# Optimization experiments

Hardware: AMD Instinct MI355X
Metric: run time of the kernel (lower is better)

The kernel has to match this reference:

```python
import jax, jax.numpy as jnp
import numpy as np

N = 20000   # nodes
E = 320000  # directed edges (before self-loops)
D = 64      # input_dim
H = 10      # GAT heads
HD = H * D  # 640
NEG_SLOPE = 0.2


def setup_inputs() -> dict:
    key = jax.random.key(0)
    ks = jax.random.split(key, 10)
    return {
        "x": jax.random.normal(ks[0], (N, D), jnp.float32),
        "W_gat": jax.random.normal(ks[1], (D, HD), jnp.float32) / np.sqrt(D).astype(np.float32),
        "att_src": jax.random.normal(ks[2], (H, D), jnp.float32) / np.sqrt(D).astype(np.float32),
        "att_dst": jax.random.normal(ks[3], (H, D), jnp.float32) / np.sqrt(D).astype(np.float32),
        "b_gat": jnp.zeros((HD,), jnp.float32),
        "W_gcn": jax.random.normal(ks[4], (HD, HD), jnp.float32) / np.sqrt(HD).astype(np.float32),
        "b_gcn": jnp.zeros((HD,), jnp.float32),
        "W1": jax.random.normal(ks[5], (2 * HD, 1500), jnp.float32) / np.sqrt(2 * HD).astype(np.float32),
        "b1": jnp.zeros((1500,), jnp.float32),
        "W2": jax.random.normal(ks[6], (1500, 10), jnp.float32) / np.sqrt(1500).astype(np.float32),
        "b2": jnp.zeros((10,), jnp.float32),
        "edge_index": jax.random.randint(ks[7], (2, E), 0, N, dtype=jnp.int64),
    }


def _forward(x, W_gat, att_src, att_dst, b_gat, W_gcn, b_gcn, W1, b1, W2, b2, edge_index):
    n = x.shape[0]
    # add self-loops (PyG default for both GATConv and GCNConv)
    loop = jnp.arange(n, dtype=edge_index.dtype)
    ei = jnp.concatenate([edge_index, jnp.stack([loop, loop])], axis=1)
    src, dst = ei[0], ei[1]

    # ---- GATConv(D -> D, heads=H, concat) ----
    xl = (x @ W_gat).reshape(n, H, D)                      # [N,H,D]
    a_src = jnp.einsum('nhd,hd->nh', xl, att_src)          # [N,H]
    a_dst = jnp.einsum('nhd,hd->nh', xl, att_dst)          # [N,H]
    alpha = jax.nn.leaky_relu(a_src[src] + a_dst[dst], NEG_SLOPE)  # [E',H]
    m = jax.ops.segment_max(alpha, dst, num_segments=n)    # segment softmax over incoming edges
    ex = jnp.exp(alpha - m[dst])
    den = jax.ops.segment_sum(ex, dst, num_segments=n)
    w = ex / (den[dst] + 1e-16)                            # [E',H]
    msg = xl[src] * w[:, :, None]                          # [E',H,D]
    x1 = jax.ops.segment_sum(msg, dst, num_segments=n).reshape(n, HD) + b_gat
    x1 = jax.nn.relu(x1)

    # ---- GCNConv(HD -> HD), symmetric norm with self-loops ----
    deg = jax.ops.segment_sum(jnp.ones(ei.shape[1], x.dtype), dst, num_segments=n)
    dinv = jnp.where(deg > 0, jax.lax.rsqrt(deg), 0.0)
    norm = dinv[src] * dinv[dst]                           # [E']
    xw = x1 @ W_gcn                                        # [N,HD]
    x2 = jax.ops.segment_sum(xw[src] * norm[:, None], dst, num_segments=n) + b_gcn
    x2 = jax.nn.relu(x2)

    # ---- global max/mean pool (batch=None -> single graph) + MLP head ----
    pooled = jnp.concatenate([x2.max(axis=0, keepdims=True),
                              x2.mean(axis=0, keepdims=True)], axis=1)  # [1, 2*HD]
    h = jax.nn.relu(pooled @ W1 + b1)
    # dropout is identity in eval mode
    return h @ W2 + b2                                     # [1, 10]


def reference(x, W_gat, att_src, att_dst, b_gat, W_gcn, b_gcn, W1, b1, W2, b2, edge_index):
    return _forward(x, W_gat, att_src, att_dst, b_gat, W_gcn, b_gcn, W1, b1, W2, b2, edge_index)
```

## Files before the change

kernel.cpp:

```cpp
#include <hip/hip_runtime.h>
#include <hip/hip_bf16.h>
#include <math.h>

#define NN 20000
#define DD 64
#define HH 10
#define HDIM 640
#define NEG 0.2f
#define H1 1500
#define BKK 128

typedef _Float16 half8 __attribute__((ext_vector_type(8)));
typedef _Float16 half4v __attribute__((ext_vector_type(4)));
typedef float f32x4 __attribute__((ext_vector_type(4)));

__global__ __launch_bounds__(256) void k_cvtB(const float* __restrict__ Wgcn,
                                              const float* __restrict__ Wg,
                                              _Float16* __restrict__ Wbt,
                                              _Float16* __restrict__ WgT)
{
    __shared__ float t[32][33];
    const int bx = blockIdx.x;
    int by = blockIdx.y;
    const float* W; _Float16* WT; int rows, cols;
    if (by < 20) { W = Wgcn; WT = Wbt; rows = HDIM; cols = HDIM; }
    else         { W = Wg;   WT = WgT; rows = DD;   cols = HDIM; by -= 20; }
    const int lx = threadIdx.x & 31, ly = threadIdx.x >> 5;
    #pragma unroll
    for (int i = ly; i < 32; i += 8)
        t[i][lx] = W[(size_t)(by * 32 + i) * cols + bx * 32 + lx];
    __syncthreads();
    #pragma unroll
    for (int j = ly; j < 32; j += 8)
        WT[(size_t)(bx * 32 + j) * rows + by * 32 + lx] = (_Float16)t[lx][j];
}

__global__ __launch_bounds__(256) void k_gemm1(
    const float* __restrict__ x, const _Float16* __restrict__ WgT,
    const float* __restrict__ att_s, const float* __restrict__ att_d,
    _Float16* __restrict__ xl, float* __restrict__ aST, float* __restrict__ aDT)
{
    __shared__ _Float16 As[128][72];
    __shared__ _Float16 Bs[64][72];
    const int tid = threadIdx.x;
    const int m0 = blockIdx.x * 128;
    const int h  = blockIdx.y;
    const int n0 = h * 64;

    {
        const int row = tid >> 1, ch = (tid & 1) * 32;
        const int gr = m0 + row;
        if (gr < NN) {
            const float* xp = &x[(size_t)gr * DD + ch];
            #pragma unroll
            for (int i = 0; i < 8; ++i) {
                const float4 v = *(const float4*)&xp[i * 4];
                half4v o = {(_Float16)v.x, (_Float16)v.y, (_Float16)v.z, (_Float16)v.w};
                *(half4v*)&As[row][ch + i * 4] = o;
            }
        } else {
            const half8 z = {0, 0, 0, 0, 0, 0, 0, 0};
            #pragma unroll
            for (int i = 0; i < 4; ++i) *(half8*)&As[row][ch + i * 8] = z;
        }
    }
    {
        const int row = tid >> 2, part = (tid & 3) * 16;
        const _Float16* wp = &WgT[(size_t)(n0 + row) * DD + part];
        *(half8*)&Bs[row][part]     = *(const half8*)&wp[0];
        *(half8*)&Bs[row][part + 8] = *(const half8*)&wp[8];
    }
    __syncthreads();

    const int lane = tid & 63, wave = tid >> 6;
    const int l15 = lane & 15, quad = lane >> 4;
    f32x4 acc[2][4];
    #pragma unroll
    for (int r = 0; r < 2; ++r)
        #pragma unroll
        for (int c = 0; c < 4; ++c) acc[r][c] = (f32x4){0.f, 0.f, 0.f, 0.f};

    #pragma unroll
    for (int ks = 0; ks < 2; ++ks) {
        const half8 a0 = *(const half8*)&As[wave * 32 + l15][ks * 32 + quad * 8];
        const half8 a1 = *(const half8*)&As[wave * 32 + 16 + l15][ks * 32 + quad * 8];
        #pragma unroll
        for (int c = 0; c < 4; ++c) {
            const half8 b = *(const half8*)&Bs[c * 16 + l15][ks * 32 + quad * 8];
            acc[0][c] = __builtin_amdgcn_mfma_f32_16x16x32_f16(a0, b, acc[0][c], 0, 0, 0);
            acc[1][c] = __builtin_amdgcn_mfma_f32_16x16x32_f16(a1, b, acc[1][c], 0, 0, 0);
        }
    }

    float asv[4], adv[4];
    #pragma unroll
    for (int c = 0; c < 4; ++c) {
        asv[c] = att_s[h * DD + c * 16 + l15];
        adv[c] = att_d[h * DD + c * 16 + l15];
    }
    #pragma unroll
    for (int r = 0; r < 2; ++r) {
        float ps[4] = {0.f, 0.f, 0.f, 0.f}, pd[4] = {0.f, 0.f, 0.f, 0.f};
        #pragma unroll
        for (int c = 0; c < 4; ++c)
            #pragma unroll
            for (int g = 0; g < 4; ++g) {
                ps[g] = fmaf(acc[r][c][g], asv[c], ps[g]);
                pd[g] = fmaf(acc[r][c][g], adv[c], pd[g]);
            }
        #pragma unroll
        for (int m = 1; m <= 8; m <<= 1)
            #pragma unroll
            for (int g = 0; g < 4; ++g) {
                ps[g] += __shfl_xor(ps[g], m);
                pd[g] += __shfl_xor(pd[g], m);
            }
        #pragma unroll
        for (int c = 0; c < 4; ++c)
            #pragma unroll
            for (int g = 0; g < 4; ++g) {
                const int row = m0 + wave * 32 + r * 16 + quad * 4 + g;
                if (row < NN)
                    xl[(size_t)row * HDIM + n0 + c * 16 + l15] = (_Float16)acc[r][c][g];
            }
        if (l15 == 0)
            #pragma unroll
            for (int g = 0; g < 4; ++g) {
                const int row = m0 + wave * 32 + r * 16 + quad * 4 + g;
                if (row < NN) {
                    aST[(size_t)h * NN + row] = ps[g];
                    aDT[(size_t)h * NN + row] = pd[g];
                }
            }
    }
}

__global__ void k_count(const int* __restrict__ ei, int E, int* __restrict__ cnt)
{
    const int e = blockIdx.x * blockDim.x + threadIdx.x;
    if (e >= E + NN) return;
    const int d = (e < E) ? ei[E + e] : (e - E);
    atomicAdd(&cnt[d], 1);
}

__global__ __launch_bounds__(1024) void k_scan(const int* __restrict__ cnt,
                                               int* __restrict__ rowptr,
                                               float* __restrict__ dinv)
{
    __shared__ int sh[1024];
    const int t = threadIdx.x;
    const int CH = 20;
    const int base = t * CH;
    int loc[CH];
    int s = 0;
    #pragma unroll
    for (int i = 0; i < CH; ++i) {
        const int idx = base + i;
        const int c = (idx < NN) ? cnt[idx] : 0;
        loc[i] = s; s += c;
    }
    sh[t] = s; __syncthreads();
    for (int off = 1; off < 1024; off <<= 1) {
        const int v = (t >= off) ? sh[t - off] : 0;
        __syncthreads();
        sh[t] += v;
        __syncthreads();
    }
    const int prev = (t == 0) ? 0 : sh[t - 1];
    #pragma unroll
    for (int i = 0; i < CH; ++i) {
        const int idx = base + i;
        if (idx < NN) {
            rowptr[idx] = prev + loc[i];
            dinv[idx]   = rsqrtf((float)cnt[idx]);
        }
    }
    if (t == 1023) rowptr[NN] = sh[1023];
}

__global__ void k_fill(const int* __restrict__ ei, int E,
                       const int* __restrict__ rowptr,
                       int* __restrict__ cursor, int* __restrict__ csr)
{
    const int e = blockIdx.x * blockDim.x + threadIdx.x;
    if (e >= E + NN) return;
    int s, d;
    if (e < E) { s = ei[e]; d = ei[E + e]; } else { s = d = e - E; }
    const int pos = atomicAdd(&cursor[d], 1);
    csr[rowptr[d] + pos] = s;
}

__device__ __forceinline__ bool slice_map3(int bid, int& s, int& m)
{
    const int r = bid & 7, k = bid >> 3;
    if (k < 625) { s = r; m = k; return true; }
    s = 8 + (r >> 2);
    m = (r & 3) * 157 + (k - 625);
    return m < 625;
}

__device__ __forceinline__ float lrexp(float a)
{
    a = (a >= 0.f) ? a : NEG * a;
    return __expf(a);
}

__global__ __launch_bounds__(256) void k_gat_gather4(
    const int* __restrict__ rowptr, const int* __restrict__ csr,
    const float* __restrict__ aST, const float* __restrict__ aDT,
    const _Float16* __restrict__ xl, const float* __restrict__ b_gat,
    _Float16* __restrict__ x1)
{
    int s, m;
    if (!slice_map3(blockIdx.x, s, m)) return;
    const int wave = threadIdx.x >> 6, lane = threadIdx.x & 63;
    const int g = lane >> 3, l = lane & 7;
    const int n = m * 32 + wave * 8 + g;
    const int col = s * 64 + l * 8;
    const float* __restrict__ as = aST + (size_t)s * NN;
    const _Float16* __restrict__ xc = xl + col;
    const float ad = aDT[(size_t)s * NN + n];

    float acc[8];
    #pragma unroll
    for (int i = 0; i < 8; ++i) acc[i] = 0.f;
    float ws = 0.f;

    const int j0 = rowptr[n], j1 = rowptr[n + 1];
    int j = j0;
    for (; j + 3 < j1; j += 4) {
        const int sA = csr[j], sB = csr[j + 1], sC = csr[j + 2], sD = csr[j + 3];
        const float wA = lrexp(as[sA] + ad);
        const float wB = lrexp(as[sB] + ad);
        const float wC = lrexp(as[sC] + ad);
        const float wD = lrexp(as[sD] + ad);
        ws += wA + wB + wC + wD;
        const half8 vA = *(const half8*)&xc[(size_t)sA * HDIM];
        const half8 vB = *(const half8*)&xc[(size_t)sB * HDIM];
        const half8 vC = *(const half8*)&xc[(size_t)sC * HDIM];
        const half8 vD = *(const half8*)&xc[(size_t)sD * HDIM];
        #pragma unroll
        for (int i = 0; i < 8; ++i) {
            acc[i] = fmaf(wA, (float)vA[i], acc[i]);
            acc[i] = fmaf(wB, (float)vB[i], acc[i]);
            acc[i] = fmaf(wC, (float)vC[i], acc[i]);
            acc[i] = fmaf(wD, (float)vD[i], acc[i]);
        }
    }
    for (; j < j1; ++j) {
        const int sA = csr[j];
        const float wA = lrexp(as[sA] + ad);
        ws += wA;
        const half8 vA = *(const half8*)&xc[(size_t)sA * HDIM];
        #pragma unroll
        for (int i = 0; i < 8; ++i) acc[i] = fmaf(wA, (float)vA[i], acc[i]);
    }

    const float rr = 1.f / (ws + 1e-16f);
    const float4 ba = *(const float4*)&b_gat[col];
    const float4 bb = *(const float4*)&b_gat[col + 4];
    const float bv[8] = {ba.x, ba.y, ba.z, ba.w, bb.x, bb.y, bb.z, bb.w};
    half8 o;
    #pragma unroll
    for (int i = 0; i < 8; ++i) {
        const float v = fmaf(acc[i], rr, bv[i]);
        o[i] = (_Float16)((v > 0.f) ? v : 0.f);
    }
    *(half8*)&x1[(size_t)n * HDIM + col] = o;
}

__global__ __launch_bounds__(256) void k_gcn_gather4(
    const int* __restrict__ rowptr, const int* __restrict__ csr,
    const float* __restrict__ dinv, const _Float16* __restrict__ x1,
    _Float16* __restrict__ t)
{
    int s, m;
    if (!slice_map3(blockIdx.x, s, m)) return;
    const int wave = threadIdx.x >> 6, lane = threadIdx.x & 63;
    const int g = lane >> 3, l = lane & 7;
    const int n = m * 32 + wave * 8 + g;
    const int col = s * 64 + l * 8;
    const _Float16* __restrict__ xc = x1 + col;
    const float dd = dinv[n];

    float acc[8];
    #pragma unroll
    for (int i = 0; i < 8; ++i) acc[i] = 0.f;

    const int j0 = rowptr[n], j1 = rowptr[n + 1];
    int j = j0;
    for (; j + 3 < j1; j += 4) {
        const int sA = csr[j], sB = csr[j + 1], sC = csr[j + 2], sD = csr[j + 3];
        const float wA = dinv[sA] * dd, wB = dinv[sB] * dd;
        const float wC = dinv[sC] * dd, wD = dinv[sD] * dd;
        const half8 vA = *(const half8*)&xc[(size_t)sA * HDIM];
        const half8 vB = *(const half8*)&xc[(size_t)sB * HDIM];
        const half8 vC = *(const half8*)&xc[(size_t)sC * HDIM];
        const half8 vD = *(const half8*)&xc[(size_t)sD * HDIM];
        #pragma unroll
        for (int i = 0; i < 8; ++i) {
            acc[i] = fmaf(wA, (float)vA[i], acc[i]);
            acc[i] = fmaf(wB, (float)vB[i], acc[i]);
            acc[i] = fmaf(wC, (float)vC[i], acc[i]);
            acc[i] = fmaf(wD, (float)vD[i], acc[i]);
        }
    }
    for (; j < j1; ++j) {
        const int sA = csr[j];
        const float wA = dinv[sA] * dd;
        const half8 vA = *(const half8*)&xc[(size_t)sA * HDIM];
        #pragma unroll
        for (int i = 0; i < 8; ++i) acc[i] = fmaf(wA, (float)vA[i], acc[i]);
    }

    half8 o;
    #pragma unroll
    for (int i = 0; i < 8; ++i) o[i] = (_Float16)acc[i];
    *(half8*)&t[(size_t)n * HDIM + col] = o;
}

__global__ __launch_bounds__(256) void k_gemm2(const _Float16* __restrict__ X,
                                               const _Float16* __restrict__ Wbt,
                                               const float* __restrict__ b_gcn,
                                               float* __restrict__ pmax,
                                               float* __restrict__ psum)
{
    __shared__ _Float16 Bs[2][128 * BKK];
    const int bid = blockIdx.x;
    const int r = bid & 7, q = bid >> 3;
    const int strip = (q / 5) * 8 + r;
    const int nt = q % 5;
    if (strip >= 157) return;

    const int tid = threadIdx.x;
    const int lane = tid & 63, wave = tid >> 6;
    const int l15 = lane & 15, quad = lane >> 4;
    const int m0 = strip * 128 + wave * 32;
    const int n0 = nt * 128;
    const int l7 = l15 & 7;
    const int jrow = lane >> 4, jchunk = lane & 15;

    f32x4 acc[2][8];
    #pragma unroll
    for (int rr = 0; rr < 2; ++rr)
        #pragma unroll
        for (int c = 0; c < 8; ++c) acc[rr][c] = (f32x4){0.f, 0.f, 0.f, 0.f};

    const _Float16* a0p = &X[(size_t)(m0 + l15) * HDIM + quad * 8];
    const _Float16* a1p = a0p + (size_t)16 * HDIM;

#define STAGE2(buf, kb)                                                          \
    {                                                                            \
        _Pragma("unroll")                                                        \
        for (int i = 0; i < 8; ++i) {                                            \
            const int rw = (wave * 8 + i) * 4 + jrow;                            \
            const int ck = jchunk ^ (rw & 7);                                    \
            const _Float16* src = &Wbt[(size_t)(n0 + rw) * HDIM + (kb) + ck * 8];\
            __builtin_amdgcn_global_load_lds(                                    \
                (const __attribute__((address_space(1))) void*)src,              \
                (__attribute__((address_space(3))) void*)&Bs[buf][(size_t)(wave * 8 + i) * 512], \
                16, 0, 0);                                                       \
        }                                                                        \
    }

    STAGE2(0, 0);
    for (int it = 0; it < 5; ++it) {
        const int kb = it * BKK;
        half8 a0[4], a1[4];
        #pragma unroll
        for (int ks = 0; ks < 4; ++ks) {
            a0[ks] = *(const half8*)(a0p + kb + ks * 32);
            a1[ks] = *(const half8*)(a1p + kb + ks * 32);
        }
        if (it < 4) {
            STAGE2((it + 1) & 1, kb + BKK);
            asm volatile("s_waitcnt vmcnt(8)" ::: "memory");
        } else {
            asm volatile("s_waitcnt vmcnt(0)" ::: "memory");
        }
        __builtin_amdgcn_s_barrier();
        const _Float16* Bsc = Bs[it & 1];
        #pragma unroll
        for (int ks = 0; ks < 4; ++ks) {
            #pragma unroll
            for (int c = 0; c < 8; ++c) {
                const int br = c * 16 + l15;
                const int ck = (4 * ks + quad) ^ l7;
                const half8 b = *(const half8*)&Bsc[(size_t)br * BKK + ck * 8];
                acc[0][c] = __builtin_amdgcn_mfma_f32_16x16x32_f16(a0[ks], b, acc[0][c], 0, 0, 0);
                acc[1][c] = __builtin_amdgcn_mfma_f32_16x16x32_f16(a1[ks], b, acc[1][c], 0, 0, 0);
            }
        }
        __builtin_amdgcn_s_barrier();
    }
#undef STAGE2

    float lmax[8], lsum[8];
    #pragma unroll
    for (int c = 0; c < 8; ++c) { lmax[c] = 0.f; lsum[c] = 0.f; }
    #pragma unroll
    for (int c = 0; c < 8; ++c) {
        const float bb = b_gcn[n0 + c * 16 + l15];
        #pragma unroll
        for (int rr = 0; rr < 2; ++rr)
            #pragma unroll
            for (int g = 0; g < 4; ++g) {
                const int row = m0 + rr * 16 + quad * 4 + g;
                if (row < NN) {
                    float v = acc[rr][c][g] + bb;
                    v = (v > 0.f) ? v : 0.f;
                    lmax[c] = fmaxf(lmax[c], v);
                    lsum[c] += v;
                }
            }
    }
    float* redm = (float*)Bs;
    float* reds = redm + 128;
    if (tid < 128) { redm[tid] = 0.f; reds[tid] = 0.f; }
    __syncthreads();
    #pragma unroll
    for (int c = 0; c < 8; ++c) {
        const int col = c * 16 + l15;
        atomicMax((int*)&redm[col], __float_as_int(lmax[c]));
        atomicAdd(&reds[col], lsum[c]);
    }
    __syncthreads();
    if (tid < 128) {
        atomicMax((int*)&pmax[n0 + tid], __float_as_int(redm[tid]));
        atomicAdd(&psum[n0 + tid], reds[tid]);
    }
}

__global__ __launch_bounds__(256) void k_mlp1(const float* __restrict__ pmax,
                                              const float* __restrict__ psum,
                                              const float* __restrict__ W1,
                                              float* __restrict__ hacc)
{
    __shared__ float pl[80];
    const int t = threadIdx.x;
    const int i0 = blockIdx.y * 80;
    if (t < 80) {
        const int i = i0 + t;
        pl[t] = (i < HDIM) ? pmax[i] : psum[i - HDIM] * (1.0f / NN);
    }
    __syncthreads();
    const int j = blockIdx.x * 256 + t;
    if (j >= H1) return;
    float acc = 0.f;
    #pragma unroll 8
    for (int i = 0; i < 80; ++i)
        acc = fmaf(pl[i], W1[(size_t)(i0 + i) * H1 + j], acc);
    atomicAdd(&hacc[j], acc);
}

__global__ __launch_bounds__(256) void k_mlp2(const float* __restrict__ hacc,
                                              const float* __restrict__ b1,
                                              const float* __restrict__ W2,
                                              const float* __restrict__ b2,
                                              float* __restrict__ out)
{
    __shared__ float hsh[H1];
    __shared__ float red[256];
    const int t = threadIdx.x;
    for (int i = t; i < H1; i += 256) {
        const float v = hacc[i] + b1[i];
        hsh[i] = (v > 0.f) ? v : 0.f;
    }
    __syncthreads();
    float acc[10];
    #pragma unroll
    for (int k = 0; k < 10; ++k) acc[k] = 0.f;
    for (int i = t; i < H1; i += 256) {
        const float h = hsh[i];
        #pragma unroll
        for (int k = 0; k < 10; ++k) acc[k] = fmaf(h, W2[i * 10 + k], acc[k]);
    }
    for (int k = 0; k < 10; ++k) {
        red[t] = acc[k]; __syncthreads();
        for (int s2 = 128; s2 > 0; s2 >>= 1) {
            if (t < s2) red[t] += red[t + s2];
            __syncthreads();
        }
        if (t == 0) out[k] = red[0] + b2[k];
        __syncthreads();
    }
}

extern "C" void kernel_launch(void* const* d_in, const int* in_sizes, int n_in,
                              void* d_out, int out_size, void* d_ws, size_t ws_size,
                              hipStream_t stream)
{
    const float* x     = (const float*)d_in[0];
    const float* Wg    = (const float*)d_in[1];
    const float* att_s = (const float*)d_in[2];
    const float* att_d = (const float*)d_in[3];
    const float* b_gat = (const float*)d_in[4];
    const float* Wgcn  = (const float*)d_in[5];
    const float* b_gcn = (const float*)d_in[6];
    const float* W1    = (const float*)d_in[7];
    const float* b1    = (const float*)d_in[8];
    const float* W2    = (const float*)d_in[9];
    const float* b2    = (const float*)d_in[10];
    const int*   ei    = (const int*)d_in[11];
    const int E = in_sizes[11] / 2;
    const int EP = E + NN;
    float* out = (float*)d_out;

    char* wsp = (char*)d_ws;
    size_t off = 0;
    auto alc = [&](size_t b) { void* p = wsp + off; off += (b + 255) & ~(size_t)255; return p; };
    _Float16* bufA = (_Float16*)alc((size_t)NN * HDIM * 2);
    _Float16* bufB = (_Float16*)alc((size_t)NN * HDIM * 2);
    float* aST    = (float*)alc((size_t)HH * NN * 4);
    float* aDT    = (float*)alc((size_t)HH * NN * 4);
    int*   rowptr = (int*)alc((size_t)(NN + 1) * 4);
    int*   csr    = (int*)alc((size_t)EP * 4);
    float* dinv   = (float*)alc((size_t)NN * 4);
    _Float16* Wbt = (_Float16*)alc((size_t)HDIM * HDIM * 2);
    _Float16* WgT = (_Float16*)alc((size_t)HDIM * DD * 2);
    const size_t zoff = off;
    int*   cnt    = (int*)alc((size_t)NN * 4);
    int*   cursor = (int*)alc((size_t)NN * 4);
    float* pmax   = (float*)alc((size_t)HDIM * 4);
    float* psum   = (float*)alc((size_t)HDIM * 4);
    float* hacc   = (float*)alc((size_t)H1 * 4);
    const size_t zsize = off - zoff;

    hipMemsetAsync(cnt, 0, zsize, stream);

    dim3 gw(HDIM / 32, HDIM / 32 + DD / 32);
    k_cvtB<<<gw, 256, 0, stream>>>(Wgcn, Wg, Wbt, WgT);
    dim3 g1((NN + 127) / 128, HH);
    k_gemm1<<<g1, 256, 0, stream>>>(x, WgT, att_s, att_d, bufA, aST, aDT);
    k_count<<<(EP + 255) / 256, 256, 0, stream>>>(ei, E, cnt);
    k_scan<<<1, 1024, 0, stream>>>(cnt, rowptr, dinv);
    k_fill<<<(EP + 255) / 256, 256, 0, stream>>>(ei, E, rowptr, cursor, csr);
    const int GG = 6256;
    k_gat_gather4<<<GG, 256, 0, stream>>>(rowptr, csr, aST, aDT, bufA, b_gat, bufB);
    k_gcn_gather4<<<GG, 256, 0, stream>>>(rowptr, csr, dinv, bufB, bufA);
    k_gemm2<<<800, 256, 0, stream>>>(bufA, Wbt, b_gcn, pmax, psum);
    dim3 gm1(6, 16);
    k_mlp1<<<gm1, 256, 0, stream>>>(pmax, psum, W1, hacc);
    k_mlp2<<<1, 256, 0, stream>>>(hacc, b1, W2, b2, out);
}
```

Measured before the change: 317.4 us.

## Widen gather per-thread columns to 16 and halve GEMM K-tile

The GAT and GCN gather kernels now give each thread 16 feature columns (two half8 loads per neighbor) with 4 lanes per node instead of 8. Each block covers 64 nodes, so the grid is roughly halved, and a bounds check is added. The aim is more bytes in flight per thread and fewer index and weight loads per column. The GCN GEMM K-tile drops from 128 to 64 with a new LDS staging layout and sched_barriers. This shrinks shared memory per block to raise occupancy, at the cost of more pipeline iterations and barriers.

```diff
diff --git a/kernel.cpp b/kernel.cpp
--- a/kernel.cpp
+++ b/kernel.cpp
@@ -8,7 +8,7 @@
 #define HDIM 640
 #define NEG 0.2f
 #define H1 1500
-#define BKK 128
+#define BKK 64
 
 typedef _Float16 half8 __attribute__((ext_vector_type(8)));
 typedef _Float16 half4v __attribute__((ext_vector_type(4)));
@@ -190,13 +190,13 @@
     csr[rowptr[d] + pos] = s;
 }
 
-__device__ __forceinline__ bool slice_map3(int bid, int& s, int& m)
+__device__ __forceinline__ bool slice_map5(int bid, int& s, int& m)
 {
     const int r = bid & 7, k = bid >> 3;
-    if (k < 625) { s = r; m = k; return true; }
+    if (k < 313) { s = r; m = k; return true; }
     s = 8 + (r >> 2);
-    m = (r & 3) * 157 + (k - 625);
-    return m < 625;
+    m = (r & 3) * 79 + (k - 313);
+    return m < 313;
 }
 
 __device__ __forceinline__ float lrexp(float a)
@@ -205,25 +205,26 @@
     return __expf(a);
 }
 
-__global__ __launch_bounds__(256) void k_gat_gather4(
+__global__ __launch_bounds__(256) void k_gat_gather5(
     const int* __restrict__ rowptr, const int* __restrict__ csr,
     const float* __restrict__ aST, const float* __restrict__ aDT,
     const _Float16* __restrict__ xl, const float* __restrict__ b_gat,
     _Float16* __restrict__ x1)
 {
     int s, m;
-    if (!slice_map3(blockIdx.x, s, m)) return;
+    if (!slice_map5(blockIdx.x, s, m)) return;
     const int wave = threadIdx.x >> 6, lane = threadIdx.x & 63;
-    const int g = lane >> 3, l = lane & 7;
-    const int n = m * 32 + wave * 8 + g;
-    const int col = s * 64 + l * 8;
+    const int g = lane >> 2, l = lane & 3;
+    const int n = m * 64 + wave * 16 + g;
+    if (n >= NN) return;
+    const int col = s * 64 + l * 16;
     const float* __restrict__ as = aST + (size_t)s * NN;
     const _Float16* __restrict__ xc = xl + col;
     const float ad = aDT[(size_t)s * NN + n];
 
-    float acc[8];
-    #pragma unroll
-    for (int i = 0; i < 8; ++i) acc[i] = 0.f;
+    float acc0[8], acc1[8];
+    #pragma unroll
+    for (int i = 0; i < 8; ++i) { acc0[i] = 0.f; acc1[i] = 0.f; }
     float ws = 0.f;
 
     const int j0 = rowptr[n], j1 = rowptr[n + 1];
@@ -235,57 +236,76 @@
         const float wC = lrexp(as[sC] + ad);
         const float wD = lrexp(as[sD] + ad);
         ws += wA + wB + wC + wD;
-        const half8 vA = *(const half8*)&xc[(size_t)sA * HDIM];
-        const half8 vB = *(const half8*)&xc[(size_t)sB * HDIM];
-        const half8 vC = *(const half8*)&xc[(size_t)sC * HDIM];
-        const half8 vD = *(const half8*)&xc[(size_t)sD * HDIM];
+        const half8 vA0 = *(const half8*)&xc[(size_t)sA * HDIM];
+        const half8 vA1 = *(const half8*)&xc[(size_t)sA * HDIM + 8];
+        const half8 vB0 = *(const half8*)&xc[(size_t)sB * HDIM];
+        const half8 vB1 = *(const half8*)&xc[(size_t)sB * HDIM + 8];
+        const half8 vC0 = *(const half8*)&xc[(size_t)sC * HDIM];
+        const half8 vC1 = *(const half8*)&xc[(size_t)sC * HDIM + 8];
+        const half8 vD0 = *(const half8*)&xc[(size_t)sD * HDIM];
+        const half8 vD1 = *(const half8*)&xc[(size_t)sD * HDIM + 8];
         #pragma unroll
         for (int i = 0; i < 8; ++i) {
-            acc[i] = fmaf(wA, (float)vA[i], acc[i]);
-            acc[i] = fmaf(wB, (float)vB[i], acc[i]);
-            acc[i] = fmaf(wC, (float)vC[i], acc[i]);
-            acc[i] = fmaf(wD, (float)vD[i], acc[i]);
+            acc0[i] = fmaf(wA, (float)vA0[i], acc0[i]);
+            acc1[i] = fmaf(wA, (float)vA1[i], acc1[i]);
+            acc0[i] = fmaf(wB, (float)vB0[i], acc0[i]);
+            acc1[i] = fmaf(wB, (float)vB1[i], acc1[i]);
+            acc0[i] = fmaf(wC, (float)vC0[i], acc0[i]);
+            acc1[i] = fmaf(wC, (float)vC1[i], acc1[i]);
+            acc0[i] = fmaf(wD, (float)vD0[i], acc0[i]);
+            acc1[i] = fmaf(wD, (float)vD1[i], acc1[i]);
         }
     }
     for (; j < j1; ++j) {
         const int sA = csr[j];
         const float wA = lrexp(as[sA] + ad);
         ws += wA;
-        const half8 vA = *(const half8*)&xc[(size_t)sA * HDIM];
-        #pragma unroll
-        for (int i = 0; i < 8; ++i) acc[i] = fmaf(wA, (float)vA[i], acc[i]);
+        const half8 vA0 = *(const half8*)&xc[(size_t)sA * HDIM];
+        const half8 vA1 = *(const half8*)&xc[(size_t)sA * HDIM + 8];
+        #pragma unroll
+        for (int i = 0; i < 8; ++i) {
+            acc0[i] = fmaf(wA, (float)vA0[i], acc0[i]);
+            acc1[i] = fmaf(wA, (float)vA1[i], acc1[i]);
+        }
     }
 
     const float rr = 1.f / (ws + 1e-16f);
     const float4 ba = *(const float4*)&b_gat[col];
     const float4 bb = *(const float4*)&b_gat[col + 4];
-    const float bv[8] = {ba.x, ba.y, ba.z, ba.w, bb.x, bb.y, bb.z, bb.w};
-    half8 o;
+    const float4 bc = *(const float4*)&b_gat[col + 8];
+    const float4 bd = *(const float4*)&b_gat[col + 12];
+    const float bv0[8] = {ba.x, ba.y, ba.z, ba.w, bb.x, bb.y, bb.z, bb.w};
+    const float bv1[8] = {bc.x, bc.y, bc.z, bc.w, bd.x, bd.y, bd.z, bd.w};
+    half8 o0, o1;
     #pragma unroll
     for (int i = 0; i < 8; ++i) {
-        const float v = fmaf(acc[i], rr, bv[i]);
-        o[i] = (_Float16)((v > 0.f) ? v : 0.f);
-    }
-    *(half8*)&x1[(size_t)n * HDIM + col] = o;
-}
-
-__global__ __launch_bounds__(256) void k_gcn_gather4(
+        const float v0 = fmaf(acc0[i], rr, bv0[i]);
+        const float v1 = fmaf(acc1[i], rr, bv1[i]);
+        o0[i] = (_Float16)((v0 > 0.f) ? v0 : 0.f);
+        o1[i] = (_Float16)((v1 > 0.f) ? v1 : 0.f);
+    }
+    *(half8*)&x1[(size_t)n * HDIM + col]     = o0;
+    *(half8*)&x1[(size_t)n * HDIM + col + 8] = o1;
+}
+
+__global__ __launch_bounds__(256) void k_gcn_gather5(
     const int* __restrict__ rowptr, const int* __restrict__ csr,
     const float* __restrict__ dinv, const _Float16* __restrict__ x1,
     _Float16* __restrict__ t)
 {
     int s, m;
-    if (!slice_map3(blockIdx.x, s, m)) return;
+    if (!slice_map5(blockIdx.x, s, m)) return;
     const int wave = threadIdx.x >> 6, lane = threadIdx.x & 63;
-    const int g = lane >> 3, l = lane & 7;
-    const int n = m * 32 + wave * 8 + g;
-    const int col = s * 64 + l * 8;
+    const int g = lane >> 2, l = lane & 3;
+    const int n = m * 64 + wave * 16 + g;
+    if (n >= NN) return;
+    const int col = s * 64 + l * 16;
     const _Float16* __restrict__ xc = x1 + col;
     const float dd = dinv[n];
 
-    float acc[8];
-    #pragma unroll
-    for (int i = 0; i < 8; ++i) acc[i] = 0.f;
+    float acc0[8], acc1[8];
+    #pragma unroll
+    for (int i = 0; i < 8; ++i) { acc0[i] = 0.f; acc1[i] = 0.f; }
 
     const int j0 = rowptr[n], j1 = rowptr[n + 1];
     int j = j0;
@@ -293,30 +313,43 @@
         const int sA = csr[j], sB = csr[j + 1], sC = csr[j + 2], sD = csr[j + 3];
         const float wA = dinv[sA] * dd, wB = dinv[sB] * dd;
         const float wC = dinv[sC] * dd, wD = dinv[sD] * dd;
-        const half8 vA = *(const half8*)&xc[(size_t)sA * HDIM];
-        const half8 vB = *(const half8*)&xc[(size_t)sB * HDIM];
-        const half8 vC = *(const half8*)&xc[(size_t)sC * HDIM];
-        const half8 vD = *(const half8*)&xc[(size_t)sD * HDIM];
+        const half8 vA0 = *(const half8*)&xc[(size_t)sA * HDIM];
+        const half8 vA1 = *(const half8*)&xc[(size_t)sA * HDIM + 8];
+        const half8 vB0 = *(const half8*)&xc[(size_t)sB * HDIM];
+        const half8 vB1 = *(const half8*)&xc[(size_t)sB * HDIM + 8];
+        const half8 vC0 = *(const half8*)&xc[(size_t)sC * HDIM];
+        const half8 vC1 = *(const half8*)&xc[(size_t)sC * HDIM + 8];
+        const half8 vD0 = *(const half8*)&xc[(size_t)sD * HDIM];
+        const half8 vD1 = *(const half8*)&xc[(size_t)sD * HDIM + 8];
         #pragma unroll
         for (int i = 0; i < 8; ++i) {
-            acc[i] = fmaf(wA, (float)vA[i], acc[i]);
-            acc[i] = fmaf(wB, (float)vB[i], acc[i]);
-            acc[i] = fmaf(wC, (float)vC[i], acc[i]);
-            acc[i] = fmaf(wD, (float)vD[i], acc[i]);
+            acc0[i] = fmaf(wA, (float)vA0[i], acc0[i]);
+            acc1[i] = fmaf(wA, (float)vA1[i], acc1[i]);
+            acc0[i] = fmaf(wB, (float)vB0[i], acc0[i]);
+            acc1[i] = fmaf(wB, (float)vB1[i], acc1[i]);
+            acc0[i] = fmaf(wC, (float)vC0[i], acc0[i]);
+            acc1[i] = fmaf(wC, (float)vC1[i], acc1[i]);
+            acc0[i] = fmaf(wD, (float)vD0[i], acc0[i]);
+            acc1[i] = fmaf(wD, (float)vD1[i], acc1[i]);
         }
     }
     for (; j < j1; ++j) {
         const int sA = csr[j];
         const float wA = dinv[sA] * dd;
-        const half8 vA = *(const half8*)&xc[(size_t)sA * HDIM];
-        #pragma unroll
-        for (int i = 0; i < 8; ++i) acc[i] = fmaf(wA, (float)vA[i], acc[i]);
-    }
-
-    half8 o;
-    #pragma unroll
-    for (int i = 0; i < 8; ++i) o[i] = (_Float16)acc[i];
-    *(half8*)&t[(size_t)n * HDIM + col] = o;
+        const half8 vA0 = *(const half8*)&xc[(size_t)sA * HDIM];
+        const half8 vA1 = *(const half8*)&xc[(size_t)sA * HDIM + 8];
+        #pragma unroll
+        for (int i = 0; i < 8; ++i) {
+            acc0[i] = fmaf(wA, (float)vA0[i], acc0[i]);
+            acc1[i] = fmaf(wA, (float)vA1[i], acc1[i]);
+        }
+    }
+
+    half8 o0, o1;
+    #pragma unroll
+    for (int i = 0; i < 8; ++i) { o0[i] = (_Float16)acc0[i]; o1[i] = (_Float16)acc1[i]; }
+    *(half8*)&t[(size_t)n * HDIM + col]     = o0;
+    *(half8*)&t[(size_t)n * HDIM + col + 8] = o1;
 }
 
 __global__ __launch_bounds__(256) void k_gemm2(const _Float16* __restrict__ X,
@@ -337,8 +370,6 @@
     const int l15 = lane & 15, quad = lane >> 4;
     const int m0 = strip * 128 + wave * 32;
     const int n0 = nt * 128;
-    const int l7 = l15 & 7;
-    const int jrow = lane >> 4, jchunk = lane & 15;
 
     f32x4 acc[2][8];
     #pragma unroll
@@ -348,52 +379,57 @@
 
     const _Float16* a0p = &X[(size_t)(m0 + l15) * HDIM + quad * 8];
     const _Float16* a1p = a0p + (size_t)16 * HDIM;
-
-#define STAGE2(buf, kb)                                                          \
+    const int srow = wave * 8 + (lane >> 3);
+    const int sck  = lane & 7;
+
+#define STAGE4(buf, kb)                                                          \
     {                                                                            \
         _Pragma("unroll")                                                        \
-        for (int i = 0; i < 8; ++i) {                                            \
-            const int rw = (wave * 8 + i) * 4 + jrow;                            \
-            const int ck = jchunk ^ (rw & 7);                                    \
+        for (int i = 0; i < 4; ++i) {                                            \
+            const int rw = i * 32 + srow;                                        \
+            const int ck = sck ^ (rw & 7);                                       \
             const _Float16* src = &Wbt[(size_t)(n0 + rw) * HDIM + (kb) + ck * 8];\
             __builtin_amdgcn_global_load_lds(                                    \
                 (const __attribute__((address_space(1))) void*)src,              \
-                (__attribute__((address_space(3))) void*)&Bs[buf][(size_t)(wave * 8 + i) * 512], \
+                (__attribute__((address_space(3))) void*)&Bs[buf][((size_t)i * 256 + tid) * 8], \
                 16, 0, 0);                                                       \
         }                                                                        \
     }
 
-    STAGE2(0, 0);
-    for (int it = 0; it < 5; ++it) {
+    STAGE4(0, 0);
+    for (int it = 0; it < 10; ++it) {
         const int kb = it * BKK;
-        half8 a0[4], a1[4];
-        #pragma unroll
-        for (int ks = 0; ks < 4; ++ks) {
+        half8 a0[2], a1[2];
+        #pragma unroll
+        for (int ks = 0; ks < 2; ++ks) {
             a0[ks] = *(const half8*)(a0p + kb + ks * 32);
             a1[ks] = *(const half8*)(a1p + kb + ks * 32);
         }
-        if (it < 4) {
-            STAGE2((it + 1) & 1, kb + BKK);
-            asm volatile("s_waitcnt vmcnt(8)" ::: "memory");
+        if (it < 9) {
+            STAGE4((it + 1) & 1, kb + BKK);
+            asm volatile("s_waitcnt vmcnt(4)" ::: "memory");
         } else {
             asm volatile("s_waitcnt vmcnt(0)" ::: "memory");
         }
         __builtin_amdgcn_s_barrier();
+        __builtin_amdgcn_sched_barrier(0);
         const _Float16* Bsc = Bs[it & 1];
         #pragma unroll
-        for (int ks = 0; ks < 4; ++ks) {
+        for (int ks = 0; ks < 2; ++ks) {
             #pragma unroll
             for (int c = 0; c < 8; ++c) {
                 const int br = c * 16 + l15;
-                const int ck = (4 * ks + quad) ^ l7;
+                const int ck = (ks * 4 + quad) ^ (br & 7);
                 const half8 b = *(const half8*)&Bsc[(size_t)br * BKK + ck * 8];
                 acc[0][c] = __builtin_amdgcn_mfma_f32_16x16x32_f16(a0[ks], b, acc[0][c], 0, 0, 0);
                 acc[1][c] = __builtin_amdgcn_mfma_f32_16x16x32_f16(a1[ks], b, acc[1][c], 0, 0, 0);
             }
         }
+        __builtin_amdgcn_sched_barrier(0);
         __builtin_amdgcn_s_barrier();
-    }
-#undef STAGE2
+        __builtin_amdgcn_sched_barrier(0);
+    }
+#undef STAGE4
 
     float lmax[8], lsum[8];
     #pragma unroll
@@ -535,9 +571,9 @@
     k_count<<<(EP + 255) / 256, 256, 0, stream>>>(ei, E, cnt);
     k_scan<<<1, 1024, 0, stream>>>(cnt, rowptr, dinv);
     k_fill<<<(EP + 255) / 256, 256, 0, stream>>>(ei, E, rowptr, cursor, csr);
-    const int GG = 6256;
-    k_gat_gather4<<<GG, 256, 0, stream>>>(rowptr, csr, aST, aDT, bufA, b_gat, bufB);
-    k_gcn_gather4<<<GG, 256, 0, stream>>>(rowptr, csr, dinv, bufB, bufA);
+    const int GG = 3136;
+    k_gat_gather5<<<GG, 256, 0, stream>>>(rowptr, csr, aST, aDT, bufA, b_gat, bufB);
+    k_gcn_gather5<<<GG, 256, 0, stream>>>(rowptr, csr, dinv, bufB, bufA);
     k_gemm2<<<800, 256, 0, stream>>>(bufA, Wbt, b_gcn, pmax, psum);
     dim3 gm1(6, 16);
     k_mlp1<<<gm1, 256, 0, stream>>>(pmax, psum, W1, hacc);
```

Result: slower. 333.6 us (+5.1%).
